# Performance work log

Hardware: AMD Instinct MI355X
Metric: run time of the kernel (lower is better)

The kernel has to match this reference:

```python
import jax, jax.numpy as jnp
import numpy as np

D, E, DFF, TOPK = 768, 4, 1024, 2


def setup_inputs() -> dict:
    key = jax.random.key(0)
    ks = jax.random.split(key, 6)
    s = 0.02  # init scale for weights
    return {
        "input_ids": jax.random.normal(ks[0], (8, 2048, D), dtype=jnp.float32),
        "W": jax.random.normal(ks[1], (D, D), dtype=jnp.float32) * s,
        "b": jnp.zeros((D,), dtype=jnp.float32),
        "Wg": jax.random.normal(ks[2], (D, E), dtype=jnp.float32) * s,
        "bg": jnp.zeros((E,), dtype=jnp.float32),
        "W1": jax.random.normal(ks[3], (E, D, DFF), dtype=jnp.float32) * s,
        "b1": jnp.zeros((E, DFF), dtype=jnp.float32),
        "W2": jax.random.normal(ks[4], (E, DFF, D), dtype=jnp.float32) * s,
        "b2": jnp.zeros((E, D), dtype=jnp.float32),
    }


def reference(input_ids, W, b, Wg, bg, W1, b1, W2, b2):
    B, S, _ = input_ids.shape
    # Dense projection feeding the MoE layer
    h = jnp.einsum("bsd,de->bse", input_ids, W) + b          # [B,S,D]
    t = h.reshape(-1, D)                                      # [T,D] tokens

    # Token-choice router: softmax over experts, top-2, renormalized gates
    logits = t @ Wg + bg                                      # [T,E]
    probs = jax.nn.softmax(logits, axis=-1)
    vals, idx = jax.lax.top_k(probs, TOPK)                    # [T,K]
    gates = vals / jnp.sum(vals, axis=-1, keepdims=True)
    # Dense combine weights [T,E]: zero for non-selected experts
    comb = jnp.sum(jax.nn.one_hot(idx, E, dtype=t.dtype) * gates[..., None], axis=1)

    # Expert FFNs (E small -> compute all experts, weighted combine)
    pre = jnp.einsum("td,edf->etf", t, W1) + b1[:, None, :]   # [E,T,DFF]
    y_e = jnp.einsum("etf,efd->etd", jax.nn.gelu(pre), W2) + b2[:, None, :]
    out = jnp.einsum("te,etd->td", comb, y_e)                 # [T,D]
    return out.reshape(B, S, D)
```

## Files before the change

### kernel.cpp

```cpp
#include <hip/hip_runtime.h>

#define DIM 768
#define NEXP 4
#define DFF_ 1024
#define CAP 16384

typedef __attribute__((ext_vector_type(4))) float f32x4;
typedef __attribute__((ext_vector_type(8))) short s16x8;

__device__ __forceinline__ unsigned short f32_to_bf16(float f) {
  unsigned int u = __float_as_uint(f);
  unsigned int r = (u + 0x7FFFu + ((u >> 16) & 1u)) >> 16;
  return (unsigned short)r;
}

__global__ void transpose_bf16_kernel(const float* __restrict__ in,
                                      unsigned short* __restrict__ out,
                                      int R, int C, int ldo, int zOut) {
  __shared__ float tile[32][33];
  const int bx = blockIdx.x, by = blockIdx.y, bz = blockIdx.z;
  in  += (size_t)bz * R * C;
  out += (size_t)bz * zOut;
  const int tx = threadIdx.x, ty = threadIdx.y;
#pragma unroll
  for (int i = 0; i < 4; i++) {
    int r = by * 32 + ty + i * 8;
    int c = bx * 32 + tx;
    tile[ty + i * 8][tx] = in[(size_t)r * C + c];
  }
  __syncthreads();
#pragma unroll
  for (int i = 0; i < 4; i++) {
    int oc = bx * 32 + ty + i * 8;
    int orow = by * 32 + tx;
    out[(size_t)oc * ldo + orow] = f32_to_bf16(tile[tx][ty + i * 8]);
  }
}

__global__ void convert_bf16_kernel(const float* __restrict__ in,
                                    unsigned short* __restrict__ out) {
  size_t i = ((size_t)blockIdx.x * 256 + threadIdx.x) * 8;
  float4 a = *(const float4*)(in + i);
  float4 b = *(const float4*)(in + i + 4);
  union { unsigned short u[8]; uint4 v; } pk;
  pk.u[0] = f32_to_bf16(a.x); pk.u[1] = f32_to_bf16(a.y);
  pk.u[2] = f32_to_bf16(a.z); pk.u[3] = f32_to_bf16(a.w);
  pk.u[4] = f32_to_bf16(b.x); pk.u[5] = f32_to_bf16(b.y);
  pk.u[6] = f32_to_bf16(b.z); pk.u[7] = f32_to_bf16(b.w);
  *(uint4*)(out + i) = pk.v;
}

__global__ void wfg_kernel(const float* __restrict__ W, const float* __restrict__ Wg,
                           const float* __restrict__ b, const float* __restrict__ bg,
                           float* __restrict__ wfg, float* __restrict__ bgp) {
  int gid = blockIdx.x * 256 + threadIdx.x;
  if (gid < DIM * NEXP) {
    int k = gid >> 2, e = gid & 3;
    const float* wr = W + (size_t)k * DIM;
    float acc = 0.f;
    for (int d = 0; d < DIM; d++) acc += wr[d] * Wg[d * NEXP + e];
    wfg[gid] = acc;
  } else if (gid < DIM * NEXP + NEXP) {
    int e = gid - DIM * NEXP;
    float acc = bg[e];
    for (int d = 0; d < DIM; d++) acc += b[d] * Wg[d * NEXP + e];
    bgp[e] = acc;
  }
}

__global__ void router_kernel(const float* __restrict__ x, const float* __restrict__ wfg,
                              const float* __restrict__ bgp, const float* __restrict__ b2,
                              int2* __restrict__ rte, float2* __restrict__ rtg,
                              float* __restrict__ out) {
  __shared__ float wfgS[DIM * NEXP];
  __shared__ float b2S[NEXP * DIM];
  const int tid = threadIdx.x;
  for (int i = tid; i < DIM * NEXP; i += 256) { wfgS[i] = wfg[i]; b2S[i] = b2[i]; }
  __syncthreads();
  const int w = tid >> 6, lane = tid & 63;
  const size_t t = (size_t)blockIdx.x * 4 + w;
  const float* xr = x + t * DIM;
  float a0 = 0.f, a1 = 0.f, a2 = 0.f, a3 = 0.f;
#pragma unroll
  for (int i = 0; i < 12; i++) {
    int k = i * 64 + lane;
    float xv = xr[k];
    a0 += xv * wfgS[k * 4 + 0];
    a1 += xv * wfgS[k * 4 + 1];
    a2 += xv * wfgS[k * 4 + 2];
    a3 += xv * wfgS[k * 4 + 3];
  }
#pragma unroll
  for (int off = 32; off > 0; off >>= 1) {
    a0 += __shfl_xor(a0, off);
    a1 += __shfl_xor(a1, off);
    a2 += __shfl_xor(a2, off);
    a3 += __shfl_xor(a3, off);
  }
  float l[NEXP] = {a0 + bgp[0], a1 + bgp[1], a2 + bgp[2], a3 + bgp[3]};
  float m = fmaxf(fmaxf(l[0], l[1]), fmaxf(l[2], l[3]));
  float p[NEXP]; float s = 0.f;
#pragma unroll
  for (int e = 0; e < NEXP; e++) { p[e] = expf(l[e] - m); s += p[e]; }
#pragma unroll
  for (int e = 0; e < NEXP; e++) p[e] /= s;
  int i1 = 0;
#pragma unroll
  for (int e = 1; e < NEXP; e++) if (p[e] > p[i1]) i1 = e;
  int i2 = -1;
#pragma unroll
  for (int e = 0; e < NEXP; e++) { if (e == i1) continue; if (i2 < 0 || p[e] > p[i2]) i2 = e; }
  float denom = p[i1] + p[i2];
  float c1 = p[i1] / denom, c2 = p[i2] / denom;
  float c[NEXP] = {0.f, 0.f, 0.f, 0.f};
  c[i1] = c1; c[i2] = c2;
  if (lane == 0) { rte[t] = make_int2(i1, i2); rtg[t] = make_float2(c1, c2); }
#pragma unroll
  for (int i = 0; i < 12; i++) {
    int n = i * 64 + lane;
    out[t * DIM + n] = c[0] * b2S[n] + c[1] * b2S[DIM + n] + c[2] * b2S[2 * DIM + n] + c[3] * b2S[3 * DIM + n];
  }
}

__global__ void assign_kernel(const int2* __restrict__ rte, const float2* __restrict__ rtg,
                              int* __restrict__ cnt, int* __restrict__ idx_tok,
                              float* __restrict__ gate_sel) {
  __shared__ int hist[NEXP];
  __shared__ int base[NEXP];
  const int tid = threadIdx.x;
  if (tid < NEXP) hist[tid] = 0;
  __syncthreads();
  const int t = blockIdx.x * 256 + tid;
  int2 e = rte[t];
  float2 g = rtg[t];
  int r1 = atomicAdd(&hist[e.x], 1);
  int r2 = atomicAdd(&hist[e.y], 1);
  __syncthreads();
  if (tid < NEXP) base[tid] = atomicAdd(&cnt[tid], hist[tid]);
  __syncthreads();
  int s1 = base[e.x] + r1, s2 = base[e.y] + r2;
  idx_tok[e.x * CAP + s1] = t;  gate_sel[e.x * CAP + s1] = g.x;
  idx_tok[e.y * CAP + s2] = t;  gate_sel[e.y * CAP + s2] = g.y;
}

template <int MODE, int CH>
__launch_bounds__(256)
__global__ void gemm_kernel(const unsigned short* __restrict__ A, const int lda,
                            const unsigned short* __restrict__ Bt, const int ldb,
                            const int K, const int N,
                            const float* __restrict__ bias,
                            const int* __restrict__ idx_tok,
                            const float* __restrict__ gate_sel,
                            const int* __restrict__ cnts,
                            unsigned short* __restrict__ outB,
                            float* __restrict__ outF, const int ldo) {
  const int lin = blockIdx.y * gridDim.x + blockIdx.x;
  const int nT = gridDim.x;
  const int xcd = lin & 7, t8 = lin >> 3;
  int bn = 0, bm0 = 0;
  int seg = 0, bmLoc = 0, cnt = 1 << 30, segBase = 0;

  if constexpr (MODE == 0) {
    const int perXcd = gridDim.y >> 3;
    const int mi = t8 % CH;
    const int rest = t8 / CH;
    bn = rest % nT;
    const int mc = rest / nT;
    bm0 = (xcd * perXcd + mc * CH + mi) * 128;
  } else {
    const int c0 = cnts[0], c1 = cnts[1], c2 = cnts[2], c3 = cnts[3];
    const int t0 = (c0 + 127) >> 7, t1 = (c1 + 127) >> 7,
              t2 = (c2 + 127) >> 7, t3 = (c3 + 127) >> 7;
    const int p1 = t0, p2 = p1 + t1, p3 = p2 + t2, tot = p3 + t3;
    const int perXcd = (tot + 7) >> 3;
    bn = t8 % nT;
    const int mloc = t8 / nT;
    if (mloc >= perXcd) return;
    const int mIdx = xcd * perXcd + mloc;
    if (mIdx >= tot) return;
    seg = (mIdx >= p2) ? ((mIdx >= p3) ? 3 : 2) : ((mIdx >= p1) ? 1 : 0);
    const int pre = (seg == 3) ? p3 : (seg == 2) ? p2 : (seg == 1) ? p1 : 0;
    bmLoc = (mIdx - pre) * 128;
    segBase = seg * CAP;
    cnt = (seg == 3) ? c3 : (seg == 2) ? c2 : (seg == 1) ? c1 : c0;
    Bt += (size_t)seg * N * ldb;
    if constexpr (MODE == 1) bias += (size_t)seg * N;
  }

  __shared__ unsigned short As[128 * 32];
  __shared__ unsigned short Bs[128 * 32];
  __shared__ int idxS[128];
  __shared__ float gateS[128];

  const int tid = threadIdx.x;
  const int w = tid >> 6;
  const int lane = tid & 63;

  if constexpr (MODE != 0) {
    if (tid < 128) {
      int r = bmLoc + tid;
      int cl = (r < cnt) ? r : bmLoc;
      idxS[tid] = idx_tok[segBase + cl];
      if constexpr (MODE == 1) gateS[tid] = gate_sel[segBase + cl];
    }
    __syncthreads();
  }

  const int r0 = tid >> 2, r1 = 64 + r0;
  const int gq = (tid & 3) ^ (r0 & 3);
  const unsigned short *aP0, *aP1;
  if constexpr (MODE == 0) {
    aP0 = A + (size_t)(bm0 + r0) * lda + gq * 8;
    aP1 = A + (size_t)(bm0 + r1) * lda + gq * 8;
  } else if constexpr (MODE == 1) {
    aP0 = A + (size_t)idxS[r0] * lda + gq * 8;
    aP1 = A + (size_t)idxS[r1] * lda + gq * 8;
  } else {
    aP0 = A + (size_t)(segBase + bmLoc + r0) * lda + gq * 8;
    aP1 = A + (size_t)(segBase + bmLoc + r1) * lda + gq * 8;
  }
  const unsigned short* bP0 = Bt + (size_t)(bn * 128 + r0) * ldb + gq * 8;
  const unsigned short* bP1 = Bt + (size_t)(bn * 128 + r1) * ldb + gq * 8;

  f32x4 acc[4][4];
#pragma unroll
  for (int i = 0; i < 4; i++)
#pragma unroll
    for (int j = 0; j < 4; j++) acc[i][j] = (f32x4){0.f, 0.f, 0.f, 0.f};

  const int quad = lane >> 4;
  const int m16 = lane & 15;
  const int wm = (w & 1) * 64;
  const int wn = (w >> 1) * 64;

  for (int k0 = 0; k0 < K; k0 += 32) {
    char* la0 = (char*)As + w * 1024;
    char* la1 = (char*)As + 4096 + w * 1024;
    char* lb0 = (char*)Bs + w * 1024;
    char* lb1 = (char*)Bs + 4096 + w * 1024;
    __builtin_amdgcn_global_load_lds((const __attribute__((address_space(1))) void*)(aP0 + k0),
                                     (__attribute__((address_space(3))) void*)la0, 16, 0, 0);
    __builtin_amdgcn_global_load_lds((const __attribute__((address_space(1))) void*)(aP1 + k0),
                                     (__attribute__((address_space(3))) void*)la1, 16, 0, 0);
    __builtin_amdgcn_global_load_lds((const __attribute__((address_space(1))) void*)(bP0 + k0),
                                     (__attribute__((address_space(3))) void*)lb0, 16, 0, 0);
    __builtin_amdgcn_global_load_lds((const __attribute__((address_space(1))) void*)(bP1 + k0),
                                     (__attribute__((address_space(3))) void*)lb1, 16, 0, 0);
    __syncthreads();
    const int sw = (quad ^ (m16 & 3)) * 16;
    s16x8 af[4], bf[4];
#pragma unroll
    for (int i = 0; i < 4; i++)
      af[i] = *(const s16x8*)((const char*)As + (wm + i * 16 + m16) * 64 + sw);
#pragma unroll
    for (int j = 0; j < 4; j++)
      bf[j] = *(const s16x8*)((const char*)Bs + (wn + j * 16 + m16) * 64 + sw);
#pragma unroll
    for (int i = 0; i < 4; i++)
#pragma unroll
      for (int j = 0; j < 4; j++)
        acc[i][j] = __builtin_amdgcn_mfma_f32_16x16x32_bf16(af[i], bf[j], acc[i][j], 0, 0, 0);
    __syncthreads();
  }

#pragma unroll
  for (int i = 0; i < 4; i++) {
    const int rloc = wm + i * 16 + quad * 4;
#pragma unroll
    for (int j = 0; j < 4; j++) {
      const int col = bn * 128 + wn + j * 16 + m16;
      if constexpr (MODE == 0) {
        float bv = bias[col];
#pragma unroll
        for (int r = 0; r < 4; r++)
          outB[(size_t)(bm0 + rloc + r) * ldo + col] = f32_to_bf16(acc[i][j][r] + bv);
      } else if constexpr (MODE == 1) {
        float bv = bias[col];
#pragma unroll
        for (int r = 0; r < 4; r++) {
          if (bmLoc + rloc + r < cnt) {
            float v = acc[i][j][r] + bv;
            float t3 = v + 0.044715f * v * v * v;
            float e2 = exp2f(t3 * 2.302208206984525f);
            float rc = __builtin_amdgcn_rcpf(1.0f + e2);
            float g = v - v * rc;
            outB[(size_t)(segBase + bmLoc + rloc + r) * ldo + col] =
                f32_to_bf16(g * gateS[rloc + r]);
          }
        }
      } else {
#pragma unroll
        for (int r = 0; r < 4; r++) {
          if (bmLoc + rloc + r < cnt) {
            int tok = idxS[rloc + r];
            atomicAdd(outF + (size_t)tok * ldo + col, acc[i][j][r]);
          }
        }
      }
    }
  }
}

extern "C" void kernel_launch(void* const* d_in, const int* in_sizes, int n_in,
                              void* d_out, int out_size, void* d_ws, size_t ws_size,
                              hipStream_t stream) {
  (void)in_sizes; (void)n_in; (void)out_size; (void)ws_size;
  const float* x  = (const float*)d_in[0];
  const float* W  = (const float*)d_in[1];
  const float* b  = (const float*)d_in[2];
  const float* Wg = (const float*)d_in[3];
  const float* bg = (const float*)d_in[4];
  const float* W1 = (const float*)d_in[5];
  const float* b1 = (const float*)d_in[6];
  const float* W2 = (const float*)d_in[7];
  const float* b2 = (const float*)d_in[8];
  float* out = (float*)d_out;
  char* ws = (char*)d_ws;

  unsigned short* tbf  = (unsigned short*)(ws + 0);
  unsigned short* w1t  = (unsigned short*)(ws + 25165824);
  unsigned short* w2t  = (unsigned short*)(ws + 31457280);
  float* wfg           = (float*)(ws + 37748736);
  float* bgp           = (float*)(ws + 37761024);
  int2*  rte           = (int2*)(ws + 37761280);
  float2* rtg          = (float2*)(ws + 37892352);
  int*   cnt           = (int*)(ws + 38023424);
  int*   idx_tok       = (int*)(ws + 38023680);
  float* gate_sel      = (float*)(ws + 38285824);
  unsigned short* g    = (unsigned short*)(ws + 38547968);
  unsigned short* xbf  = (unsigned short*)(ws + 38547968);
  unsigned short* wt   = (unsigned short*)(ws + 63713792);

  hipMemsetAsync(cnt, 0, NEXP * sizeof(int), stream);
  transpose_bf16_kernel<<<dim3(24, 24, 1), dim3(32, 8), 0, stream>>>(W, wt, 768, 768, 768, 589824);
  transpose_bf16_kernel<<<dim3(32, 24, 4), dim3(32, 8), 0, stream>>>(W1, w1t, 768, 1024, 768, 786432);
  transpose_bf16_kernel<<<dim3(24, 32, 4), dim3(32, 8), 0, stream>>>(W2, w2t, 1024, 768, 1024, 786432);
  convert_bf16_kernel<<<6144, 256, 0, stream>>>(x, xbf);
  wfg_kernel<<<13, 256, 0, stream>>>(W, Wg, b, bg, wfg, bgp);
  router_kernel<<<4096, 256, 0, stream>>>(x, wfg, bgp, b2, rte, rtg, out);
  assign_kernel<<<64, 256, 0, stream>>>(rte, rtg, cnt, idx_tok, gate_sel);

  gemm_kernel<0, 8><<<dim3(6, 128), 256, 0, stream>>>(
      xbf, 768, wt, 768, 768, 768, b, nullptr, nullptr, nullptr, tbf, nullptr, 768);
  gemm_kernel<1, 8><<<dim3(8, 264), 256, 0, stream>>>(
      tbf, 768, w1t, 768, 768, 1024, b1, idx_tok, gate_sel, cnt, g, nullptr, 1024);
  gemm_kernel<2, 8><<<dim3(6, 264), 256, 0, stream>>>(
      g, 1024, w2t, 1024, 1024, 768, nullptr, idx_tok, nullptr, cnt, nullptr, out, 768);
}
```

Before: 462.5 us.

## Replace atomic scatter-add in expert down-projection with bf16 store plus gather-combine kernel

The second expert GEMM no longer scatters fp32 atomicAdds into the output by token. It now writes bf16 rows to a packed per-expert buffer. A new combine kernel gathers each token's two expert rows through a token-to-slot map recorded in the assign kernel, then adds the gate-weighted b2 bias. Because the router no longer initializes the output with bias, it skips that full-tensor write. This trades atomic contention and read-modify-write traffic for an extra bf16 intermediate write/read, an extra launch, and an additional bf16 rounding of the expert outputs.

Result: faster. 429.8 us (-7.1%).

```diff
diff --git a/kernel.cpp b/kernel.cpp
--- a/kernel.cpp
+++ b/kernel.cpp
@@ -12,6 +12,9 @@
   unsigned int u = __float_as_uint(f);
   unsigned int r = (u + 0x7FFFu + ((u >> 16) & 1u)) >> 16;
   return (unsigned short)r;
+}
+__device__ __forceinline__ float bf16_to_f32(unsigned short u) {
+  return __uint_as_float(((unsigned int)u) << 16);
 }
 
 __global__ void transpose_bf16_kernel(const float* __restrict__ in,
@@ -69,13 +72,11 @@
 }
 
 __global__ void router_kernel(const float* __restrict__ x, const float* __restrict__ wfg,
-                              const float* __restrict__ bgp, const float* __restrict__ b2,
-                              int2* __restrict__ rte, float2* __restrict__ rtg,
-                              float* __restrict__ out) {
+                              const float* __restrict__ bgp,
+                              int2* __restrict__ rte, float2* __restrict__ rtg) {
   __shared__ float wfgS[DIM * NEXP];
-  __shared__ float b2S[NEXP * DIM];
   const int tid = threadIdx.x;
-  for (int i = tid; i < DIM * NEXP; i += 256) { wfgS[i] = wfg[i]; b2S[i] = b2[i]; }
+  for (int i = tid; i < DIM * NEXP; i += 256) wfgS[i] = wfg[i];
   __syncthreads();
   const int w = tid >> 6, lane = tid & 63;
   const size_t t = (size_t)blockIdx.x * 4 + w;
@@ -97,34 +98,29 @@
     a2 += __shfl_xor(a2, off);
     a3 += __shfl_xor(a3, off);
   }
-  float l[NEXP] = {a0 + bgp[0], a1 + bgp[1], a2 + bgp[2], a3 + bgp[3]};
-  float m = fmaxf(fmaxf(l[0], l[1]), fmaxf(l[2], l[3]));
-  float p[NEXP]; float s = 0.f;
-#pragma unroll
-  for (int e = 0; e < NEXP; e++) { p[e] = expf(l[e] - m); s += p[e]; }
-#pragma unroll
-  for (int e = 0; e < NEXP; e++) p[e] /= s;
-  int i1 = 0;
-#pragma unroll
-  for (int e = 1; e < NEXP; e++) if (p[e] > p[i1]) i1 = e;
-  int i2 = -1;
-#pragma unroll
-  for (int e = 0; e < NEXP; e++) { if (e == i1) continue; if (i2 < 0 || p[e] > p[i2]) i2 = e; }
-  float denom = p[i1] + p[i2];
-  float c1 = p[i1] / denom, c2 = p[i2] / denom;
-  float c[NEXP] = {0.f, 0.f, 0.f, 0.f};
-  c[i1] = c1; c[i2] = c2;
-  if (lane == 0) { rte[t] = make_int2(i1, i2); rtg[t] = make_float2(c1, c2); }
-#pragma unroll
-  for (int i = 0; i < 12; i++) {
-    int n = i * 64 + lane;
-    out[t * DIM + n] = c[0] * b2S[n] + c[1] * b2S[DIM + n] + c[2] * b2S[2 * DIM + n] + c[3] * b2S[3 * DIM + n];
+  if (lane == 0) {
+    float l[NEXP] = {a0 + bgp[0], a1 + bgp[1], a2 + bgp[2], a3 + bgp[3]};
+    float m = fmaxf(fmaxf(l[0], l[1]), fmaxf(l[2], l[3]));
+    float p[NEXP]; float s = 0.f;
+#pragma unroll
+    for (int e = 0; e < NEXP; e++) { p[e] = expf(l[e] - m); s += p[e]; }
+#pragma unroll
+    for (int e = 0; e < NEXP; e++) p[e] /= s;
+    int i1 = 0;
+#pragma unroll
+    for (int e = 1; e < NEXP; e++) if (p[e] > p[i1]) i1 = e;
+    int i2 = -1;
+#pragma unroll
+    for (int e = 0; e < NEXP; e++) { if (e == i1) continue; if (i2 < 0 || p[e] > p[i2]) i2 = e; }
+    float denom = p[i1] + p[i2];
+    rte[t] = make_int2(i1, i2);
+    rtg[t] = make_float2(p[i1] / denom, p[i2] / denom);
   }
 }
 
 __global__ void assign_kernel(const int2* __restrict__ rte, const float2* __restrict__ rtg,
                               int* __restrict__ cnt, int* __restrict__ idx_tok,
-                              float* __restrict__ gate_sel) {
+                              float* __restrict__ gate_sel, int2* __restrict__ tok_slot) {
   __shared__ int hist[NEXP];
   __shared__ int base[NEXP];
   const int tid = threadIdx.x;
@@ -141,6 +137,37 @@
   int s1 = base[e.x] + r1, s2 = base[e.y] + r2;
   idx_tok[e.x * CAP + s1] = t;  gate_sel[e.x * CAP + s1] = g.x;
   idx_tok[e.y * CAP + s2] = t;  gate_sel[e.y * CAP + s2] = g.y;
+  tok_slot[t] = make_int2((e.x << 14) | s1, (e.y << 14) | s2);
+}
+
+__global__ void combine_kernel(const unsigned short* __restrict__ y,
+                               const int2* __restrict__ tok_slot,
+                               const float2* __restrict__ rtg,
+                               const int* __restrict__ cnts,
+                               const float* __restrict__ b2,
+                               float* __restrict__ out) {
+  __shared__ float b2S[NEXP * DIM];
+  const int tid = threadIdx.x;
+  for (int i = tid; i < NEXP * DIM; i += 256) b2S[i] = b2[i];
+  const int t0 = (cnts[0] + 127) >> 7, t1 = (cnts[1] + 127) >> 7, t2 = (cnts[2] + 127) >> 7;
+  const int rb[NEXP] = {0, t0 * 128, (t0 + t1) * 128, (t0 + t1 + t2) * 128};
+  __syncthreads();
+  const int w = tid >> 6, lane = tid & 63;
+  const size_t t = (size_t)blockIdx.x * 4 + w;
+  int2 v = tok_slot[t];
+  float2 cg = rtg[t];
+  const int e1 = v.x >> 14, s1 = v.x & (CAP - 1);
+  const int e2 = v.y >> 14, s2 = v.y & (CAP - 1);
+  const unsigned short* y1 = y + (size_t)(rb[e1] + s1) * DIM;
+  const unsigned short* y2 = y + (size_t)(rb[e2] + s2) * DIM;
+  float* op = out + t * DIM;
+  const float* bp1 = b2S + e1 * DIM;
+  const float* bp2 = b2S + e2 * DIM;
+#pragma unroll
+  for (int k = 0; k < 12; k++) {
+    int n = k * 64 + lane;
+    op[n] = bf16_to_f32(y1[n]) + bf16_to_f32(y2[n]) + cg.x * bp1[n] + cg.y * bp2[n];
+  }
 }
 
 template <int MODE, int CH>
@@ -152,13 +179,12 @@
                             const int* __restrict__ idx_tok,
                             const float* __restrict__ gate_sel,
                             const int* __restrict__ cnts,
-                            unsigned short* __restrict__ outB,
-                            float* __restrict__ outF, const int ldo) {
+                            unsigned short* __restrict__ outB, const int ldo) {
   const int lin = blockIdx.y * gridDim.x + blockIdx.x;
   const int nT = gridDim.x;
   const int xcd = lin & 7, t8 = lin >> 3;
   int bn = 0, bm0 = 0;
-  int seg = 0, bmLoc = 0, cnt = 1 << 30, segBase = 0;
+  int bmLoc = 0, cnt = 1 << 30, segBase = 0, gRow0 = 0;
 
   if constexpr (MODE == 0) {
     const int perXcd = gridDim.y >> 3;
@@ -178,10 +204,11 @@
     if (mloc >= perXcd) return;
     const int mIdx = xcd * perXcd + mloc;
     if (mIdx >= tot) return;
-    seg = (mIdx >= p2) ? ((mIdx >= p3) ? 3 : 2) : ((mIdx >= p1) ? 1 : 0);
+    const int seg = (mIdx >= p2) ? ((mIdx >= p3) ? 3 : 2) : ((mIdx >= p1) ? 1 : 0);
     const int pre = (seg == 3) ? p3 : (seg == 2) ? p2 : (seg == 1) ? p1 : 0;
     bmLoc = (mIdx - pre) * 128;
     segBase = seg * CAP;
+    gRow0 = mIdx * 128;
     cnt = (seg == 3) ? c3 : (seg == 2) ? c2 : (seg == 1) ? c1 : c0;
     Bt += (size_t)seg * N * ldb;
     if constexpr (MODE == 1) bias += (size_t)seg * N;
@@ -196,12 +223,12 @@
   const int w = tid >> 6;
   const int lane = tid & 63;
 
-  if constexpr (MODE != 0) {
+  if constexpr (MODE == 1) {
     if (tid < 128) {
       int r = bmLoc + tid;
       int cl = (r < cnt) ? r : bmLoc;
       idxS[tid] = idx_tok[segBase + cl];
-      if constexpr (MODE == 1) gateS[tid] = gate_sel[segBase + cl];
+      gateS[tid] = gate_sel[segBase + cl];
     }
     __syncthreads();
   }
@@ -216,8 +243,8 @@
     aP0 = A + (size_t)idxS[r0] * lda + gq * 8;
     aP1 = A + (size_t)idxS[r1] * lda + gq * 8;
   } else {
-    aP0 = A + (size_t)(segBase + bmLoc + r0) * lda + gq * 8;
-    aP1 = A + (size_t)(segBase + bmLoc + r1) * lda + gq * 8;
+    aP0 = A + (size_t)(gRow0 + r0) * lda + gq * 8;
+    aP1 = A + (size_t)(gRow0 + r1) * lda + gq * 8;
   }
   const unsigned short* bP0 = Bt + (size_t)(bn * 128 + r0) * ldb + gq * 8;
   const unsigned short* bP1 = Bt + (size_t)(bn * 128 + r1) * ldb + gq * 8;
@@ -284,17 +311,14 @@
             float e2 = exp2f(t3 * 2.302208206984525f);
             float rc = __builtin_amdgcn_rcpf(1.0f + e2);
             float g = v - v * rc;
-            outB[(size_t)(segBase + bmLoc + rloc + r) * ldo + col] =
-                f32_to_bf16(g * gateS[rloc + r]);
+            outB[(size_t)(gRow0 + rloc + r) * ldo + col] = f32_to_bf16(g * gateS[rloc + r]);
           }
         }
       } else {
 #pragma unroll
         for (int r = 0; r < 4; r++) {
-          if (bmLoc + rloc + r < cnt) {
-            int tok = idxS[rloc + r];
-            atomicAdd(outF + (size_t)tok * ldo + col, acc[i][j][r]);
-          }
+          if (bmLoc + rloc + r < cnt)
+            outB[(size_t)(gRow0 + rloc + r) * ldo + col] = f32_to_bf16(acc[i][j][r]);
         }
       }
     }
@@ -327,9 +351,11 @@
   int*   cnt           = (int*)(ws + 38023424);
   int*   idx_tok       = (int*)(ws + 38023680);
   float* gate_sel      = (float*)(ws + 38285824);
-  unsigned short* g    = (unsigned short*)(ws + 38547968);
-  unsigned short* xbf  = (unsigned short*)(ws + 38547968);
-  unsigned short* wt   = (unsigned short*)(ws + 63713792);
+  int2*  tok_slot      = (int2*)(ws + 38547968);
+  unsigned short* g    = (unsigned short*)(ws + 38679040);
+  unsigned short* xbf  = (unsigned short*)(ws + 38679040);
+  unsigned short* wt   = (unsigned short*)(ws + 63844864);
+  unsigned short* y    = (unsigned short*)(ws + 106574336);
 
   hipMemsetAsync(cnt, 0, NEXP * sizeof(int), stream);
   transpose_bf16_kernel<<<dim3(24, 24, 1), dim3(32, 8), 0, stream>>>(W, wt, 768, 768, 768, 589824);
@@ -337,13 +363,14 @@
   transpose_bf16_kernel<<<dim3(24, 32, 4), dim3(32, 8), 0, stream>>>(W2, w2t, 1024, 768, 1024, 786432);
   convert_bf16_kernel<<<6144, 256, 0, stream>>>(x, xbf);
   wfg_kernel<<<13, 256, 0, stream>>>(W, Wg, b, bg, wfg, bgp);
-  router_kernel<<<4096, 256, 0, stream>>>(x, wfg, bgp, b2, rte, rtg, out);
-  assign_kernel<<<64, 256, 0, stream>>>(rte, rtg, cnt, idx_tok, gate_sel);
+  router_kernel<<<4096, 256, 0, stream>>>(x, wfg, bgp, rte, rtg);
+  assign_kernel<<<64, 256, 0, stream>>>(rte, rtg, cnt, idx_tok, gate_sel, tok_slot);
 
   gemm_kernel<0, 8><<<dim3(6, 128), 256, 0, stream>>>(
-      xbf, 768, wt, 768, 768, 768, b, nullptr, nullptr, nullptr, tbf, nullptr, 768);
+      xbf, 768, wt, 768, 768, 768, b, nullptr, nullptr, nullptr, tbf, 768);
   gemm_kernel<1, 8><<<dim3(8, 264), 256, 0, stream>>>(
-      tbf, 768, w1t, 768, 768, 1024, b1, idx_tok, gate_sel, cnt, g, nullptr, 1024);
+      tbf, 768, w1t, 768, 768, 1024, b1, idx_tok, gate_sel, cnt, g, 1024);
   gemm_kernel<2, 8><<<dim3(6, 264), 256, 0, stream>>>(
-      g, 1024, w2t, 1024, 1024, 768, nullptr, idx_tok, nullptr, cnt, nullptr, out, 768);
-}
+      g, 1024, w2t, 1024, 1024, 768, nullptr, nullptr, nullptr, cnt, y, 768);
+  combine_kernel<<<4096, 256, 0, stream>>>(y, tok_slot, rtg, cnt, b2, out);
+}
```
